# Optimization experiments

Hardware: AMD Instinct MI355X
Metric: run time of the kernel (lower is better)

## Reference

```python
import jax, jax.numpy as jnp
from jax import lax
import numpy as np

RPN_BBOX_STD_DEV = np.array([0.1, 0.1, 0.2, 0.2], dtype=np.float32)
PRE_NMS_LIMIT = 2048      # anchors kept before NMS (sorted by score)
NUM_PROPOSAL = 1000       # post-NMS proposal count (init kwarg num_proposal)
NMS_THRESHOLD = 0.7       # init kwarg nms_threshold


def setup_inputs() -> dict:
    key = jax.random.key(0)
    k1, k2, k3, k4, k5, k6 = jax.random.split(key, 6)
    B, N = 4, 1_000_000
    rpn_probs = jax.random.uniform(k1, (B, N, 2), dtype=jnp.float32)
    rpn_bbox = jax.random.normal(k2, (B, N, 4), dtype=jnp.float32)
    # well-formed normalized anchors (y1, x1, y2, x2)
    cy = jax.random.uniform(k3, (B, N), dtype=jnp.float32)
    cx = jax.random.uniform(k4, (B, N), dtype=jnp.float32)
    h = jax.random.uniform(k5, (B, N), dtype=jnp.float32) * 0.25 + 0.05
    w = jax.random.uniform(k6, (B, N), dtype=jnp.float32) * 0.25 + 0.05
    anchors = jnp.stack([cy - 0.5 * h, cx - 0.5 * w, cy + 0.5 * h, cx + 0.5 * w], axis=-1)
    return {"rpn_probs": rpn_probs, "rpn_bbox": rpn_bbox, "anchors": anchors}


def apply_box_deltas(boxes, deltas):
    # boxes: (..., 4) as (y1, x1, y2, x2); deltas: (dy, dx, log(dh), log(dw))
    h = boxes[..., 2] - boxes[..., 0]
    w = boxes[..., 3] - boxes[..., 1]
    cy = boxes[..., 0] + 0.5 * h + deltas[..., 0] * h
    cx = boxes[..., 1] + 0.5 * w + deltas[..., 1] * w
    h = h * jnp.exp(deltas[..., 2])
    w = w * jnp.exp(deltas[..., 3])
    return jnp.stack([cy - 0.5 * h, cx - 0.5 * w, cy + 0.5 * h, cx + 0.5 * w], axis=-1)


def pairwise_iou(boxes):
    # boxes: (P, 4) -> (P, P)
    y1, x1, y2, x2 = boxes[:, 0], boxes[:, 1], boxes[:, 2], boxes[:, 3]
    area = (y2 - y1) * (x2 - x1)
    ih = jnp.maximum(jnp.minimum(y2[:, None], y2[None, :]) - jnp.maximum(y1[:, None], y1[None, :]), 0.0)
    iw = jnp.maximum(jnp.minimum(x2[:, None], x2[None, :]) - jnp.maximum(x1[:, None], x1[None, :]), 0.0)
    inter = ih * iw
    union = area[:, None] + area[None, :] - inter
    return inter / (union + 1e-8)


def nms_single(boxes):
    # boxes (P, 4) sorted by score desc; greedy NMS then pad/clip to NUM_PROPOSAL
    P = boxes.shape[0]
    iou = pairwise_iou(boxes)
    idx = jnp.arange(P)

    def body(keep, i):
        suppress = keep[i] & (iou[i] > NMS_THRESHOLD) & (idx > i)
        return keep & ~suppress, None

    keep, _ = lax.scan(body, jnp.ones((P,), jnp.bool_), idx)
    rank = jnp.cumsum(keep) - 1                      # position among kept boxes
    valid = keep & (rank < NUM_PROPOSAL)
    pos = jnp.where(valid, rank, NUM_PROPOSAL)       # overflow row dropped below
    out = jnp.zeros((NUM_PROPOSAL + 1, 4), boxes.dtype).at[pos].set(
        jnp.where(valid[:, None], boxes, 0.0))
    return out[:NUM_PROPOSAL]


def reference(rpn_probs, rpn_bbox, anchors):
    scores = rpn_probs[:, :, 1]                                  # foreground prob (B, N)
    deltas = rpn_bbox * jnp.asarray(RPN_BBOX_STD_DEV)
    _, ix = lax.top_k(scores, PRE_NMS_LIMIT)                     # (B, P)
    deltas_top = jnp.take_along_axis(deltas, ix[..., None], axis=1)
    anchors_top = jnp.take_along_axis(anchors, ix[..., None], axis=1)
    boxes = apply_box_deltas(anchors_top, deltas_top)            # (B, P, 4)
    boxes = jnp.clip(boxes, 0.0, 1.0)                            # clip to [0,1] window
    proposals = jax.vmap(nms_single)(boxes)                      # (B, NUM_PROPOSAL, 4)
    return proposals
```

## Files before the change

### kernel.cpp

```cpp
#include <hip/hip_runtime.h>

#define B_ 4
#define N_ 1000000
#define K_ 2048
#define P_ 1000
#define CAP_ 8192
#define THR_ 0.7f
#define NF4_ 500000
#define META_STRIDE 32
#define TILE_ 512
#define NCH_ (CAP_ / TILE_)

#define OFF_HIST 0
#define OFF_META 1048576
#define OFF_COARSE (OFF_META + 1024)
#define OFF_CAND (OFF_COARSE + 4096)
#define OFF_TOPI (OFF_CAND + 262144)
#define OFF_BOX  (OFF_TOPI + 32768)
#define OFF_MASK (OFF_BOX + 131072)

__device__ __forceinline__ unsigned fkey(float f) {
  unsigned u = __float_as_uint(f);
  return (u & 0x80000000u) ? ~u : (u | 0x80000000u);
}

__device__ __forceinline__ unsigned long long readlane64(unsigned long long v, int l) {
  unsigned lo = (unsigned)__builtin_amdgcn_readlane((int)(unsigned)(v & 0xffffffffull), l);
  unsigned hi = (unsigned)__builtin_amdgcn_readlane((int)(unsigned)(v >> 32), l);
  return ((unsigned long long)hi << 32) | (unsigned long long)lo;
}

#define PIN16(k) asm volatile("" : "+v"(k[0]), "+v"(k[1]), "+v"(k[2]), "+v"(k[3]), \
                                   "+v"(k[4]), "+v"(k[5]), "+v"(k[6]), "+v"(k[7]), \
                                   "+v"(k[8]), "+v"(k[9]), "+v"(k[10]), "+v"(k[11]), \
                                   "+v"(k[12]), "+v"(k[13]), "+v"(k[14]), "+v"(k[15]))

__global__ void __launch_bounds__(1024) hist_kernel(const float4* __restrict__ probs4,
                                                    unsigned* __restrict__ hist) {
  int b = blockIdx.y;
  __shared__ unsigned h[32768];
  for (int i = threadIdx.x; i < 32768; i += 1024) h[i] = 0u;
  __syncthreads();
  const float4* p4 = probs4 + (size_t)b * NF4_;
  int base = blockIdx.x * 8192;
  float4 v[8];
#pragma unroll
  for (int c = 0; c < 8; ++c) {
    int i4 = base + c * 1024 + threadIdx.x;
    v[c] = (i4 < NF4_) ? p4[i4] : make_float4(0.f, 0.f, 0.f, 0.f);
  }
  unsigned k[16];
#pragma unroll
  for (int c = 0; c < 8; ++c) { k[2 * c] = fkey(v[c].y) >> 16; k[2 * c + 1] = fkey(v[c].w) >> 16; }
  PIN16(k);
#pragma unroll
  for (int c = 0; c < 8; ++c) {
    int i4 = base + c * 1024 + threadIdx.x;
    if (i4 < NF4_) {
      unsigned b0 = k[2 * c], b1 = k[2 * c + 1];
      atomicAdd(&h[b0 >> 1], 1u << ((b0 & 1u) << 4));
      atomicAdd(&h[b1 >> 1], 1u << ((b1 & 1u) << 4));
    }
  }
  __syncthreads();
  unsigned* g = hist + ((size_t)b << 16);
  for (int w = threadIdx.x; w < 32768; w += 1024) {
    unsigned x = h[w];
    if (x) {
      unsigned c0 = x & 0xFFFFu, c1 = x >> 16;
      if (c0) atomicAdd(&g[2 * w], c0);
      if (c1) atomicAdd(&g[2 * w + 1], c1);
    }
  }
}

__global__ void __launch_bounds__(64) coarse_kernel(const unsigned* __restrict__ hist,
                                                    unsigned* __restrict__ coarse) {
  int b = blockIdx.y, g = blockIdx.x, lane = threadIdx.x;
  const uint4* h4 = (const uint4*)(hist + (((size_t)b) << 16) + ((size_t)g << 8));
  uint4 v = h4[lane];
  unsigned s = v.x + v.y + v.z + v.w;
#pragma unroll
  for (int off = 32; off >= 1; off >>= 1) s += __shfl_xor(s, off, 64);
  if (lane == 0) coarse[b * 256 + g] = s;
}

__global__ void select_kernel(const unsigned* __restrict__ hist, const unsigned* __restrict__ coarse,
                              unsigned* __restrict__ meta) {
  int b = blockIdx.x, t = threadIdx.x;
  __shared__ unsigned suf[256];
  __shared__ int tc_s;
  __shared__ unsigned above_s;
  const unsigned* g = hist + ((size_t)b << 16);
  suf[t] = coarse[b * 256 + t];
  __syncthreads();
  for (int off = 1; off < 256; off <<= 1) {
    unsigned add = (t + off < 256) ? suf[t + off] : 0u;
    __syncthreads();
    suf[t] += add;
    __syncthreads();
  }
  unsigned nxt = (t < 255) ? suf[t + 1] : 0u;
  if (suf[t] >= K_ && (t == 255 || nxt < K_)) { tc_s = t; above_s = nxt; }
  __syncthreads();
  int tc = tc_s;
  unsigned above = above_s;
  unsigned bs = g[tc * 256 + t];
  __syncthreads();
  suf[t] = bs;
  __syncthreads();
  for (int off = 1; off < 256; off <<= 1) {
    unsigned add = (t + off < 256) ? suf[t + off] : 0u;
    __syncthreads();
    suf[t] += add;
    __syncthreads();
  }
  unsigned nxt2 = (t < 255) ? suf[t + 1] : 0u;
  if (above + suf[t] >= K_ && (t == 255 || above + nxt2 < K_))
    meta[b * META_STRIDE + 0] = (unsigned)(tc * 256 + t);
}

__global__ void __launch_bounds__(256) compact_kernel(const float4* __restrict__ probs4,
                                                      unsigned* __restrict__ meta,
                                                      uint2* __restrict__ cand) {
  int b = blockIdx.y;
  __shared__ unsigned lcnt, gbase_s;
  __shared__ uint2 buf[4096];
  if (threadIdx.x == 0) lcnt = 0u;
  __syncthreads();
  unsigned cb = meta[b * META_STRIDE + 0];
  const float4* p4 = probs4 + (size_t)b * NF4_;
  int base = blockIdx.x * 2048;
  int lane = threadIdx.x & 63;
  float4 v[8];
#pragma unroll
  for (int c = 0; c < 8; ++c) {
    int i4 = base + c * 256 + threadIdx.x;
    v[c] = (i4 < NF4_) ? p4[i4] : make_float4(0.f, 0.f, 0.f, 0.f);
  }
  unsigned k[16];
#pragma unroll
  for (int c = 0; c < 8; ++c) { k[2 * c] = fkey(v[c].y); k[2 * c + 1] = fkey(v[c].w); }
  PIN16(k);
#pragma unroll
  for (int c = 0; c < 8; ++c) {
#pragma unroll
    for (int s = 0; s < 2; ++s) {
      int i4 = base + c * 256 + threadIdx.x;
      unsigned key = k[2 * c + s];
      bool pass = (i4 < NF4_) && ((key >> 16) >= cb);
      unsigned long long m = __ballot(pass);
      if (m) {
        int leader = __ffsll(m) - 1;
        unsigned wbase = 0;
        if (lane == leader) wbase = atomicAdd(&lcnt, (unsigned)__popcll(m));
        wbase = __shfl(wbase, leader, 64);
        if (pass) {
          unsigned pos = wbase + (unsigned)__popcll(m & ((1ull << lane) - 1ull));
          buf[pos] = make_uint2(key, (unsigned)(2 * i4 + s));
        }
      }
    }
  }
  __syncthreads();
  unsigned cnt = lcnt;
  if (threadIdx.x == 0) gbase_s = atomicAdd(&meta[b * META_STRIDE + 1], cnt);
  __syncthreads();
  unsigned gbase = gbase_s;
  for (unsigned i = threadIdx.x; i < cnt; i += 256) {
    unsigned pos = gbase + i;
    if (pos < CAP_) cand[(size_t)b * CAP_ + pos] = buf[i];
  }
}

__global__ void __launch_bounds__(256) rank_kernel(const uint2* __restrict__ cand,
                                                   const unsigned* __restrict__ meta,
                                                   unsigned* __restrict__ partial) {
  int b = blockIdx.z;
  unsigned M = meta[b * META_STRIDE + 1];
  if (M > CAP_) M = CAP_;
  unsigned tb = blockIdx.y * TILE_;
  if (tb >= M) return;
  if ((unsigned)(blockIdx.x * 256) >= M) return;
  __shared__ __align__(16) uint2 tile[TILE_];
  unsigned n = M - tb;
  if (n > TILE_) n = TILE_;
  for (unsigned t = threadIdx.x; t < n; t += 256) tile[t] = cand[(size_t)b * CAP_ + tb + t];
  int ci = blockIdx.x * 256 + threadIdx.x;
  bool act = ci < (int)M;
  uint2 me = make_uint2(0u, 0u);
  if (act) me = cand[(size_t)b * CAP_ + ci];
  unsigned long long my = ((unsigned long long)me.x << 32) | (unsigned long long)(unsigned)(~me.y);
  __syncthreads();
  if (act) {
    unsigned rank = 0;
    unsigned n2 = n >> 1;
    const uint4* t4 = (const uint4*)tile;
    for (unsigned j = 0; j < n2; ++j) {
      uint4 v = t4[j];
      unsigned long long c0 = ((unsigned long long)v.x << 32) | (unsigned long long)(unsigned)(~v.y);
      unsigned long long c1 = ((unsigned long long)v.z << 32) | (unsigned long long)(unsigned)(~v.w);
      rank += (unsigned)(c0 > my) + (unsigned)(c1 > my);
    }
    if (n & 1) {
      uint2 v = tile[n - 1];
      unsigned long long c0 = ((unsigned long long)v.x << 32) | (unsigned long long)(unsigned)(~v.y);
      rank += (unsigned)(c0 > my);
    }
    partial[((size_t)b * NCH_ + blockIdx.y) * CAP_ + ci] = rank;
  }
}

__global__ void __launch_bounds__(256) scatter_kernel(const uint2* __restrict__ cand,
                                                      const unsigned* __restrict__ meta,
                                                      const unsigned* __restrict__ partial,
                                                      const float4* __restrict__ bbox,
                                                      const float4* __restrict__ anch,
                                                      float4* __restrict__ boxes) {
  int b = blockIdx.y;
  unsigned M = meta[b * META_STRIDE + 1];
  if (M > CAP_) M = CAP_;
  unsigned ci = blockIdx.x * 256 + threadIdx.x;
  if (ci >= M) return;
  unsigned nch = (M + TILE_ - 1) / TILE_;
  const unsigned* pp = partial + (size_t)b * NCH_ * CAP_ + ci;
  unsigned rank = 0;
  for (unsigned c = 0; c < nch; ++c) rank += pp[(size_t)c * CAP_];
  if (rank >= K_) return;
  unsigned idx = cand[(size_t)b * CAP_ + ci].y;
  size_t base = (size_t)b * N_ + idx;
  float4 a = anch[base];
  float4 d = bbox[base];
  float d0 = d.x * 0.1f, d1 = d.y * 0.1f, d2 = d.z * 0.2f, d3 = d.w * 0.2f;
  float h = a.z - a.x, w = a.w - a.y;
  float cy = (a.x + 0.5f * h) + d0 * h;
  float cx = (a.y + 0.5f * w) + d1 * w;
  float h2 = h * expf(d2);
  float w2 = w * expf(d3);
  float y1 = cy - 0.5f * h2, x1 = cx - 0.5f * w2;
  float y2 = cy + 0.5f * h2, x2 = cx + 0.5f * w2;
  y1 = fminf(fmaxf(y1, 0.f), 1.f);
  x1 = fminf(fmaxf(x1, 0.f), 1.f);
  y2 = fminf(fmaxf(y2, 0.f), 1.f);
  x2 = fminf(fmaxf(x2, 0.f), 1.f);
  boxes[(b << 11) + rank] = make_float4(y1, x1, y2, x2);
}

__global__ void mask_kernel(const float4* __restrict__ boxes, unsigned long long* __restrict__ mask) {
  int wid = blockIdx.x * 4 + (threadIdx.x >> 6);
  int lane = threadIdx.x & 63;
  int b = wid >> 12;
  int rb = (wid >> 5) & 127;
  int jb = wid & 31;
  if (jb < (rb >> 2)) return;
  int j = (jb << 6) + lane;
  float4 bj = boxes[(b << 11) + j];
  float areaJ = (bj.z - bj.x) * (bj.w - bj.y);
#pragma unroll
  for (int r = 0; r < 16; ++r) {
    int i = (rb << 4) + r;
    float4 bi = boxes[(b << 11) + i];
    float areaI = (bi.z - bi.x) * (bi.w - bi.y);
    float yA = fmaxf(bi.x, bj.x), xA = fmaxf(bi.y, bj.y);
    float yB = fminf(bi.z, bj.z), xB = fminf(bi.w, bj.w);
    float ih = fmaxf(yB - yA, 0.f), iw = fmaxf(xB - xA, 0.f);
    float inter = ih * iw;
    float uni = areaI + areaJ - inter;
    float iou = inter / (uni + 1e-8f);
    bool pred = (iou > THR_) && (j > i);
    unsigned long long bits = __ballot(pred);
    if (lane == 0) mask[((size_t)((b << 11) + i) << 5) + jb] = bits;
  }
}

__global__ void __launch_bounds__(64) nms_kernel(const unsigned long long* __restrict__ mask,
                                                 const float4* __restrict__ boxes,
                                                 float4* __restrict__ out) {
  int b = blockIdx.x;
  int lane = threadIdx.x;
  __shared__ unsigned long long rows[64][33];
  __shared__ unsigned long long keptm[32];
  __shared__ int pre[32];
  __shared__ short sel[P_];
  if (lane < 32) keptm[lane] = 0ull;
  for (int r = lane; r < P_; r += 64) sel[r] = -1;
  int w = lane & 31, half = lane >> 5;
  const unsigned long long* mbase = mask + (((size_t)(b << 11)) << 5);
  unsigned long long r0[32];
#pragma unroll
  for (int j = 0; j < 32; ++j) r0[j] = mbase[j * 64 + lane];
#pragma unroll
  for (int j = 0; j < 32; ++j) rows[2 * j + half][w] = r0[j];
  __syncthreads();
  unsigned long long rem = 0ull;
  int cnt = 0;
  for (int c = 0; c < 32; ++c) {
    bool pf = (c < 31) && (w > c);
    if (pf) {
      const unsigned long long* srcN = mbase + (((size_t)(c + 1)) << 11);
#pragma unroll
      for (int j = 0; j < 32; ++j) r0[j] = srcN[j * 64 + lane];
    }
    unsigned long long rin = rows[lane][c];
    unsigned long long cur = readlane64(rem, c);
    unsigned long long kept = 0ull;
#pragma unroll
    for (int k2 = 0; k2 < 64; ++k2) {
      unsigned long long rk = readlane64(rin, k2);
      unsigned long long alive = ((cur >> k2) & 1ull) ^ 1ull;
      cur |= rk & (0ull - alive);
      kept |= alive << k2;
    }
    if (lane == 0) keptm[c] = kept;
    cnt += (int)__popcll(kept);
    if (cnt >= P_) break;
    if (w > c) {
      unsigned long long acc = 0ull;
#pragma unroll
      for (int k2 = 0; k2 < 32; ++k2) {
        int row = half * 32 + k2;
        acc |= rows[row][w] & (0ull - ((kept >> row) & 1ull));
      }
      acc |= __shfl_xor(acc, 32, 64);
      rem |= acc;
    }
    if (pf) {
#pragma unroll
      for (int j = 0; j < 32; ++j) rows[2 * j + half][w] = r0[j];
    }
    __syncthreads();
  }
  __syncthreads();
  if (lane == 0) {
    int run = 0;
    for (int c = 0; c < 32; ++c) { pre[c] = run; run += (int)__popcll(keptm[c]); }
  }
  __syncthreads();
  for (int i = lane; i < K_; i += 64) {
    int c = i >> 6, k2 = i & 63;
    unsigned long long km = keptm[c];
    if ((km >> k2) & 1ull) {
      int rank = pre[c] + (int)__popcll(km & ((1ull << k2) - 1ull));
      if (rank < P_) sel[rank] = (short)i;
    }
  }
  __syncthreads();
  for (int r = lane; r < P_; r += 64) {
    int i = sel[r];
    float4 v = make_float4(0.f, 0.f, 0.f, 0.f);
    if (i >= 0) v = boxes[(b << 11) + i];
    out[b * P_ + r] = v;
  }
}

extern "C" void kernel_launch(void* const* d_in, const int* in_sizes, int n_in,
                              void* d_out, int out_size, void* d_ws, size_t ws_size,
                              hipStream_t stream) {
  const float4* probs4 = (const float4*)d_in[0];
  const float4* bbox   = (const float4*)d_in[1];
  const float4* anch   = (const float4*)d_in[2];
  char* ws = (char*)d_ws;
  unsigned* hist = (unsigned*)(ws + OFF_HIST);
  unsigned* meta = (unsigned*)(ws + OFF_META);
  unsigned* coarse = (unsigned*)(ws + OFF_COARSE);
  uint2* cand = (uint2*)(ws + OFF_CAND);
  float4* boxes = (float4*)(ws + OFF_BOX);
  unsigned long long* mask = (unsigned long long*)(ws + OFF_MASK);
  unsigned* partial = (unsigned*)(ws + OFF_MASK);
  float4* out = (float4*)d_out;

  hipMemsetAsync(ws, 0, OFF_COARSE, stream);

  hist_kernel<<<dim3(62, B_), 1024, 0, stream>>>(probs4, hist);
  coarse_kernel<<<dim3(256, B_), 64, 0, stream>>>(hist, coarse);
  select_kernel<<<B_, 256, 0, stream>>>(hist, coarse, meta);
  compact_kernel<<<dim3(245, B_), 256, 0, stream>>>(probs4, meta, cand);
  rank_kernel<<<dim3(CAP_ / 256, NCH_, B_), 256, 0, stream>>>(cand, meta, partial);
  scatter_kernel<<<dim3(CAP_ / 256, B_), 256, 0, stream>>>(cand, meta, partial, bbox, anch, boxes);
  mask_kernel<<<(B_ * 128 * 32) / 4, 256, 0, stream>>>(boxes, mask);
  nms_kernel<<<B_, 64, 0, stream>>>(mask, boxes, out);
}
```

Baseline: 255.1 us.

## Parallelize NMS sweep across four waves with double-buffered rows and sparse resolve

The NMS kernel grows from one wave to four. Each wave now prefetches 8 mask rows instead of 32, and the chunk rows are double-buffered in shared memory. Inside a chunk, the serial 64-step resolve is replaced by a ballot over nonzero rows that visits only rows with suppression bits. The running suppression state moves to shared memory and is updated with atomicOr from all waves. The cost is an extra block-wide barrier per chunk and some shared-memory atomics.

```diff
diff --git a/kernel.cpp b/kernel.cpp
--- a/kernel.cpp
+++ b/kernel.cpp
@@ -273,70 +273,87 @@
   }
 }
 
-__global__ void __launch_bounds__(64) nms_kernel(const unsigned long long* __restrict__ mask,
-                                                 const float4* __restrict__ boxes,
-                                                 float4* __restrict__ out) {
+__global__ void __launch_bounds__(256) nms_kernel(const unsigned long long* __restrict__ mask,
+                                                  const float4* __restrict__ boxes,
+                                                  float4* __restrict__ out) {
   int b = blockIdx.x;
-  int lane = threadIdx.x;
-  __shared__ unsigned long long rows[64][33];
+  int t = threadIdx.x;
+  int wid = t >> 6, lane = t & 63;
+  int w = lane & 31, half = lane >> 5;
+  __shared__ unsigned long long rows[2][64][33];
+  __shared__ unsigned long long remS[32];
   __shared__ unsigned long long keptm[32];
   __shared__ int pre[32];
   __shared__ short sel[P_];
-  if (lane < 32) keptm[lane] = 0ull;
-  for (int r = lane; r < P_; r += 64) sel[r] = -1;
-  int w = lane & 31, half = lane >> 5;
+  __shared__ int stopF;
+  if (t < 32) { remS[t] = 0ull; keptm[t] = 0ull; }
+  if (t == 0) stopF = 0;
+  for (int r = t; r < P_; r += 256) sel[r] = -1;
   const unsigned long long* mbase = mask + (((size_t)(b << 11)) << 5);
-  unsigned long long r0[32];
-#pragma unroll
-  for (int j = 0; j < 32; ++j) r0[j] = mbase[j * 64 + lane];
-#pragma unroll
-  for (int j = 0; j < 32; ++j) rows[2 * j + half][w] = r0[j];
-  __syncthreads();
-  unsigned long long rem = 0ull;
+  unsigned long long r0[8];
+  int rowb = 2 * wid + half;
+#pragma unroll
+  for (int j = 0; j < 8; ++j) r0[j] = mbase[j * 256 + t];
+#pragma unroll
+  for (int j = 0; j < 8; ++j) rows[0][8 * j + rowb][w] = r0[j];
+  __syncthreads();
+  int cb = 0;
   int cnt = 0;
   for (int c = 0; c < 32; ++c) {
     bool pf = (c < 31) && (w > c);
     if (pf) {
       const unsigned long long* srcN = mbase + (((size_t)(c + 1)) << 11);
 #pragma unroll
-      for (int j = 0; j < 32; ++j) r0[j] = srcN[j * 64 + lane];
-    }
-    unsigned long long rin = rows[lane][c];
-    unsigned long long cur = readlane64(rem, c);
-    unsigned long long kept = 0ull;
-#pragma unroll
-    for (int k2 = 0; k2 < 64; ++k2) {
-      unsigned long long rk = readlane64(rin, k2);
-      unsigned long long alive = ((cur >> k2) & 1ull) ^ 1ull;
-      cur |= rk & (0ull - alive);
-      kept |= alive << k2;
-    }
-    if (lane == 0) keptm[c] = kept;
-    cnt += (int)__popcll(kept);
-    if (cnt >= P_) break;
+      for (int j = 0; j < 8; ++j) r0[j] = srcN[j * 256 + t];
+    }
+    if (wid == 0) {
+      unsigned long long rin = rows[cb][lane][c];
+      unsigned long long cur = remS[c];
+      unsigned long long bm = __ballot(rin != 0ull);
+      while (bm) {
+        int k2 = __ffsll((long long)bm) - 1;
+        bm &= bm - 1;
+        if (!((cur >> k2) & 1ull)) cur |= readlane64(rin, k2);
+      }
+      unsigned long long kept = ~cur;
+      cnt += (int)__popcll(kept);
+      if (lane == 0) {
+        keptm[c] = kept;
+        if (cnt >= P_) stopF = 1;
+      }
+    }
+    __syncthreads();
+    if (stopF) break;
     if (w > c) {
+      unsigned long long kept = keptm[c];
       unsigned long long acc = 0ull;
 #pragma unroll
-      for (int k2 = 0; k2 < 32; ++k2) {
-        int row = half * 32 + k2;
-        acc |= rows[row][w] & (0ull - ((kept >> row) & 1ull));
+      for (int j = 0; j < 8; ++j) {
+        int row = 8 * j + rowb;
+        acc |= rows[cb][row][w] & (0ull - ((kept >> row) & 1ull));
       }
       acc |= __shfl_xor(acc, 32, 64);
-      rem |= acc;
+      if (half == 0) {
+        unsigned lo = (unsigned)acc, hi = (unsigned)(acc >> 32);
+        unsigned* rp = (unsigned*)&remS[w];
+        if (lo) atomicOr(rp, lo);
+        if (hi) atomicOr(rp + 1, hi);
+      }
     }
     if (pf) {
 #pragma unroll
-      for (int j = 0; j < 32; ++j) rows[2 * j + half][w] = r0[j];
-    }
-    __syncthreads();
-  }
-  __syncthreads();
-  if (lane == 0) {
+      for (int j = 0; j < 8; ++j) rows[cb ^ 1][8 * j + rowb][w] = r0[j];
+    }
+    __syncthreads();
+    cb ^= 1;
+  }
+  __syncthreads();
+  if (t == 0) {
     int run = 0;
     for (int c = 0; c < 32; ++c) { pre[c] = run; run += (int)__popcll(keptm[c]); }
   }
   __syncthreads();
-  for (int i = lane; i < K_; i += 64) {
+  for (int i = t; i < K_; i += 256) {
     int c = i >> 6, k2 = i & 63;
     unsigned long long km = keptm[c];
     if ((km >> k2) & 1ull) {
@@ -345,7 +362,7 @@
     }
   }
   __syncthreads();
-  for (int r = lane; r < P_; r += 64) {
+  for (int r = t; r < P_; r += 256) {
     int i = sel[r];
     float4 v = make_float4(0.f, 0.f, 0.f, 0.f);
     if (i >= 0) v = boxes[(b << 11) + i];
@@ -378,5 +395,5 @@
   rank_kernel<<<dim3(CAP_ / 256, NCH_, B_), 256, 0, stream>>>(cand, meta, partial);
   scatter_kernel<<<dim3(CAP_ / 256, B_), 256, 0, stream>>>(cand, meta, partial, bbox, anch, boxes);
   mask_kernel<<<(B_ * 128 * 32) / 4, 256, 0, stream>>>(boxes, mask);
-  nms_kernel<<<B_, 64, 0, stream>>>(mask, boxes, out);
-}
+  nms_kernel<<<B_, 256, 0, stream>>>(mask, boxes, out);
+}
```

Result: faster. 218.3 us (-14.4%).

## Shrink radix histogram, drop coarse pass, make NMS sparse over suppressing rows

Applied to the files above, without the earlier changes.

The histogram is cut to 16K clamped bins packed as 16-bit pairs, which removes the coarse kernel and shrinks the memset. The mask matrix is zeroed inside the hist kernel. The mask kernel now writes only nonzero words and records per-row 'any suppression' bits. NMS walks only rows that can suppress something, instead of scanning all 2048 rows bit by bit. This trades fewer launches and less serial work for some atomics, and bins are coarse near the clamp boundaries. Clamping keys below 0x8000 is fine because all probabilities are non-negative.

```diff
diff --git a/kernel.cpp b/kernel.cpp
--- a/kernel.cpp
+++ b/kernel.cpp
@@ -12,16 +12,22 @@
 #define NCH_ (CAP_ / TILE_)
 
 #define OFF_HIST 0
-#define OFF_META 1048576
-#define OFF_COARSE (OFF_META + 1024)
-#define OFF_CAND (OFF_COARSE + 4096)
-#define OFF_TOPI (OFF_CAND + 262144)
-#define OFF_BOX  (OFF_TOPI + 32768)
-#define OFF_MASK (OFF_BOX + 131072)
+#define OFF_META 131072
+#define OFF_ROWANY 132096
+#define OFF_CAND 133120
+#define OFF_BOX  395264
+#define OFF_MASK 526336
+#define OFF_PART 2623488
 
 __device__ __forceinline__ unsigned fkey(float f) {
   unsigned u = __float_as_uint(f);
   return (u & 0x80000000u) ? ~u : (u | 0x80000000u);
+}
+
+__device__ __forceinline__ int b16of(unsigned key) {
+  int x = (int)(key >> 16) - 0x8000;
+  x = x < 0 ? 0 : x;
+  return x > 0x3FFF ? 0x3FFF : x;
 }
 
 __device__ __forceinline__ unsigned long long readlane64(unsigned long long v, int l) {
@@ -35,27 +41,38 @@
                                    "+v"(k[8]), "+v"(k[9]), "+v"(k[10]), "+v"(k[11]), \
                                    "+v"(k[12]), "+v"(k[13]), "+v"(k[14]), "+v"(k[15]))
 
-__global__ void __launch_bounds__(1024) hist_kernel(const float4* __restrict__ probs4,
-                                                    unsigned* __restrict__ hist) {
+__global__ void __launch_bounds__(512) hist_kernel(const float4* __restrict__ probs4,
+                                                   unsigned* __restrict__ hist,
+                                                   uint4* __restrict__ maskz) {
   int b = blockIdx.y;
-  __shared__ unsigned h[32768];
-  for (int i = threadIdx.x; i < 32768; i += 1024) h[i] = 0u;
+  __shared__ unsigned h[8192];
+  for (int i = threadIdx.x; i < 8192; i += 512) h[i] = 0u;
+  {
+    unsigned gid = (unsigned)(b * 124 + blockIdx.x);
+    if (threadIdx.x < 320u) {
+      unsigned zi = gid * 320u + threadIdx.x;
+      if (zi < 131072u) maskz[zi] = make_uint4(0u, 0u, 0u, 0u);
+    }
+  }
   __syncthreads();
   const float4* p4 = probs4 + (size_t)b * NF4_;
-  int base = blockIdx.x * 8192;
+  int base = blockIdx.x * 4096;
   float4 v[8];
 #pragma unroll
   for (int c = 0; c < 8; ++c) {
-    int i4 = base + c * 1024 + threadIdx.x;
+    int i4 = base + c * 512 + threadIdx.x;
     v[c] = (i4 < NF4_) ? p4[i4] : make_float4(0.f, 0.f, 0.f, 0.f);
   }
   unsigned k[16];
 #pragma unroll
-  for (int c = 0; c < 8; ++c) { k[2 * c] = fkey(v[c].y) >> 16; k[2 * c + 1] = fkey(v[c].w) >> 16; }
+  for (int c = 0; c < 8; ++c) {
+    k[2 * c] = (unsigned)b16of(fkey(v[c].y));
+    k[2 * c + 1] = (unsigned)b16of(fkey(v[c].w));
+  }
   PIN16(k);
 #pragma unroll
   for (int c = 0; c < 8; ++c) {
-    int i4 = base + c * 1024 + threadIdx.x;
+    int i4 = base + c * 512 + threadIdx.x;
     if (i4 < NF4_) {
       unsigned b0 = k[2 * c], b1 = k[2 * c + 1];
       atomicAdd(&h[b0 >> 1], 1u << ((b0 & 1u) << 4));
@@ -63,49 +80,49 @@
     }
   }
   __syncthreads();
-  unsigned* g = hist + ((size_t)b << 16);
-  for (int w = threadIdx.x; w < 32768; w += 1024) {
+  unsigned* g = hist + b * 8192;
+  for (int w = threadIdx.x; w < 8192; w += 512) {
     unsigned x = h[w];
-    if (x) {
-      unsigned c0 = x & 0xFFFFu, c1 = x >> 16;
-      if (c0) atomicAdd(&g[2 * w], c0);
-      if (c1) atomicAdd(&g[2 * w + 1], c1);
-    }
-  }
-}
-
-__global__ void __launch_bounds__(64) coarse_kernel(const unsigned* __restrict__ hist,
-                                                    unsigned* __restrict__ coarse) {
-  int b = blockIdx.y, g = blockIdx.x, lane = threadIdx.x;
-  const uint4* h4 = (const uint4*)(hist + (((size_t)b) << 16) + ((size_t)g << 8));
-  uint4 v = h4[lane];
-  unsigned s = v.x + v.y + v.z + v.w;
-#pragma unroll
-  for (int off = 32; off >= 1; off >>= 1) s += __shfl_xor(s, off, 64);
-  if (lane == 0) coarse[b * 256 + g] = s;
-}
-
-__global__ void select_kernel(const unsigned* __restrict__ hist, const unsigned* __restrict__ coarse,
-                              unsigned* __restrict__ meta) {
+    if (x) atomicAdd(&g[w], x);
+  }
+}
+
+__global__ void select_kernel(const unsigned* __restrict__ hist, unsigned* __restrict__ meta) {
   int b = blockIdx.x, t = threadIdx.x;
+  const unsigned* g = hist + b * 8192;
+  __shared__ unsigned part[256];
+  __shared__ unsigned gsum[64];
   __shared__ unsigned suf[256];
   __shared__ int tc_s;
   __shared__ unsigned above_s;
-  const unsigned* g = hist + ((size_t)b << 16);
-  suf[t] = coarse[b * 256 + t];
-  __syncthreads();
-  for (int off = 1; off < 256; off <<= 1) {
-    unsigned add = (t + off < 256) ? suf[t + off] : 0u;
-    __syncthreads();
-    suf[t] += add;
-    __syncthreads();
-  }
-  unsigned nxt = (t < 255) ? suf[t + 1] : 0u;
-  if (suf[t] >= K_ && (t == 255 || nxt < K_)) { tc_s = t; above_s = nxt; }
+  {
+    int grp = t >> 2, q = t & 3;
+    const unsigned* p = g + grp * 128 + q * 32;
+    unsigned s = 0;
+#pragma unroll 8
+    for (int i = 0; i < 32; ++i) { unsigned x = p[i]; s += (x & 0xFFFFu) + (x >> 16); }
+    part[t] = s;
+  }
+  __syncthreads();
+  if (t < 64) gsum[t] = part[4 * t] + part[4 * t + 1] + part[4 * t + 2] + part[4 * t + 3];
+  __syncthreads();
+  if (t < 64) suf[t] = gsum[t];
+  __syncthreads();
+  for (int off = 1; off < 64; off <<= 1) {
+    unsigned add = (t < 64 && t + off < 64) ? suf[t + off] : 0u;
+    __syncthreads();
+    if (t < 64) suf[t] += add;
+    __syncthreads();
+  }
+  if (t < 64) {
+    unsigned nxt = (t < 63) ? suf[t + 1] : 0u;
+    if (suf[t] >= K_ && (t == 63 || nxt < K_)) { tc_s = t; above_s = nxt; }
+  }
   __syncthreads();
   int tc = tc_s;
   unsigned above = above_s;
-  unsigned bs = g[tc * 256 + t];
+  unsigned wv = g[tc * 128 + (t >> 1)];
+  unsigned bs = (t & 1) ? (wv >> 16) : (wv & 0xFFFFu);
   __syncthreads();
   suf[t] = bs;
   __syncthreads();
@@ -128,7 +145,7 @@
   __shared__ uint2 buf[4096];
   if (threadIdx.x == 0) lcnt = 0u;
   __syncthreads();
-  unsigned cb = meta[b * META_STRIDE + 0];
+  int cb = (int)meta[b * META_STRIDE + 0];
   const float4* p4 = probs4 + (size_t)b * NF4_;
   int base = blockIdx.x * 2048;
   int lane = threadIdx.x & 63;
@@ -148,7 +165,7 @@
     for (int s = 0; s < 2; ++s) {
       int i4 = base + c * 256 + threadIdx.x;
       unsigned key = k[2 * c + s];
-      bool pass = (i4 < NF4_) && ((key >> 16) >= cb);
+      bool pass = (i4 < NF4_) && (b16of(key) >= cb);
       unsigned long long m = __ballot(pass);
       if (m) {
         int leader = __ffsll(m) - 1;
@@ -246,7 +263,8 @@
   boxes[(b << 11) + rank] = make_float4(y1, x1, y2, x2);
 }
 
-__global__ void mask_kernel(const float4* __restrict__ boxes, unsigned long long* __restrict__ mask) {
+__global__ void mask_kernel(const float4* __restrict__ boxes, unsigned long long* __restrict__ mask,
+                            unsigned long long* __restrict__ rowAny) {
   int wid = blockIdx.x * 4 + (threadIdx.x >> 6);
   int lane = threadIdx.x & 63;
   int b = wid >> 12;
@@ -269,76 +287,81 @@
     float iou = inter / (uni + 1e-8f);
     bool pred = (iou > THR_) && (j > i);
     unsigned long long bits = __ballot(pred);
-    if (lane == 0) mask[((size_t)((b << 11) + i) << 5) + jb] = bits;
+    if (bits && lane == 0) {
+      mask[((size_t)((b << 11) + i) << 5) + jb] = bits;
+      atomicOr(&rowAny[b * 32 + (i >> 6)], 1ull << (i & 63));
+    }
   }
 }
 
 __global__ void __launch_bounds__(64) nms_kernel(const unsigned long long* __restrict__ mask,
+                                                 const unsigned long long* __restrict__ rowAny,
                                                  const float4* __restrict__ boxes,
                                                  float4* __restrict__ out) {
   int b = blockIdx.x;
   int lane = threadIdx.x;
-  __shared__ unsigned long long rows[64][33];
-  __shared__ unsigned long long keptm[32];
+  int w = lane & 31;
+  __shared__ unsigned long long rowsBuf[256][32];
+  __shared__ unsigned short evRow[2048];
+  __shared__ unsigned long long keptw[32];
   __shared__ int pre[32];
   __shared__ short sel[P_];
-  if (lane < 32) keptm[lane] = 0ull;
   for (int r = lane; r < P_; r += 64) sel[r] = -1;
-  int w = lane & 31, half = lane >> 5;
-  const unsigned long long* mbase = mask + (((size_t)(b << 11)) << 5);
-  unsigned long long r0[32];
-#pragma unroll
-  for (int j = 0; j < 32; ++j) r0[j] = mbase[j * 64 + lane];
-#pragma unroll
-  for (int j = 0; j < 32; ++j) rows[2 * j + half][w] = r0[j];
-  __syncthreads();
-  unsigned long long rem = 0ull;
-  int cnt = 0;
-  for (int c = 0; c < 32; ++c) {
-    bool pf = (c < 31) && (w > c);
-    if (pf) {
-      const unsigned long long* srcN = mbase + (((size_t)(c + 1)) << 11);
-#pragma unroll
-      for (int j = 0; j < 32; ++j) r0[j] = srcN[j * 64 + lane];
-    }
-    unsigned long long rin = rows[lane][c];
-    unsigned long long cur = readlane64(rem, c);
-    unsigned long long kept = 0ull;
-#pragma unroll
-    for (int k2 = 0; k2 < 64; ++k2) {
-      unsigned long long rk = readlane64(rin, k2);
-      unsigned long long alive = ((cur >> k2) & 1ull) ^ 1ull;
-      cur |= rk & (0ull - alive);
-      kept |= alive << k2;
-    }
-    if (lane == 0) keptm[c] = kept;
-    cnt += (int)__popcll(kept);
-    if (cnt >= P_) break;
-    if (w > c) {
-      unsigned long long acc = 0ull;
-#pragma unroll
-      for (int k2 = 0; k2 < 32; ++k2) {
-        int row = half * 32 + k2;
-        acc |= rows[row][w] & (0ull - ((kept >> row) & 1ull));
-      }
-      acc |= __shfl_xor(acc, 32, 64);
-      rem |= acc;
-    }
-    if (pf) {
-#pragma unroll
-      for (int j = 0; j < 32; ++j) rows[2 * j + half][w] = r0[j];
-    }
-    __syncthreads();
-  }
+  unsigned long long anyv = (lane < 32) ? rowAny[b * 32 + lane] : 0ull;
+  unsigned pc = (unsigned)__popcll(anyv);
+  unsigned pref = pc;
+#pragma unroll
+  for (int off = 1; off < 32; off <<= 1) {
+    unsigned tv = __shfl_up(pref, off, 64);
+    if ((lane & 31) >= off) pref += tv;
+  }
+  int E = __shfl((int)pref, 31, 64);
+  if (lane < 32) {
+    unsigned o = pref - pc;
+    unsigned long long bm = anyv;
+    while (bm) {
+      int i = __ffsll((long long)bm) - 1;
+      bm &= bm - 1;
+      evRow[o++] = (unsigned short)((lane << 6) + i);
+    }
+  }
+  __syncthreads();
+  unsigned long long sup = 0ull;
+  const unsigned long long* mb = mask + (((size_t)(b << 11)) << 5);
+  for (int eb = 0; eb < E; eb += 256) {
+    int ne = E - eb;
+    if (ne > 256) ne = 256;
+    for (int k = (lane >> 5); k < ne; k += 2) {
+      int r = evRow[eb + k];
+      rowsBuf[k][w] = mb[((size_t)r << 5) + w];
+    }
+    __syncthreads();
+    int i0 = evRow[eb];
+    unsigned long long v0 = rowsBuf[0][w];
+    int i1 = 0;
+    unsigned long long v1 = 0ull;
+    if (ne > 1) { i1 = evRow[eb + 1]; v1 = rowsBuf[1][w]; }
+    for (int e = 0; e < ne; ++e) {
+      int i2 = 0;
+      unsigned long long v2 = 0ull;
+      if (e + 2 < ne) { i2 = evRow[eb + e + 2]; v2 = rowsBuf[e + 2][w]; }
+      int wi = i0 >> 6;
+      unsigned long long sw = readlane64(sup, wi);
+      if (!((sw >> (i0 & 63)) & 1ull)) sup |= v0;
+      i0 = i1; v0 = v1; i1 = i2; v1 = v2;
+    }
+    __syncthreads();
+  }
+  if (lane < 32) keptw[lane] = ~sup;
   __syncthreads();
   if (lane == 0) {
     int run = 0;
-    for (int c = 0; c < 32; ++c) { pre[c] = run; run += (int)__popcll(keptm[c]); }
+    for (int c = 0; c < 32; ++c) { pre[c] = run; run += (int)__popcll(keptw[c]); }
   }
   __syncthreads();
   for (int i = lane; i < K_; i += 64) {
     int c = i >> 6, k2 = i & 63;
-    unsigned long long km = keptm[c];
+    unsigned long long km = keptw[c];
     if ((km >> k2) & 1ull) {
       int rank = pre[c] + (int)__popcll(km & ((1ull << k2) - 1ull));
       if (rank < P_) sel[rank] = (short)i;
@@ -362,21 +385,20 @@
   char* ws = (char*)d_ws;
   unsigned* hist = (unsigned*)(ws + OFF_HIST);
   unsigned* meta = (unsigned*)(ws + OFF_META);
-  unsigned* coarse = (unsigned*)(ws + OFF_COARSE);
+  unsigned long long* rowAny = (unsigned long long*)(ws + OFF_ROWANY);
   uint2* cand = (uint2*)(ws + OFF_CAND);
   float4* boxes = (float4*)(ws + OFF_BOX);
   unsigned long long* mask = (unsigned long long*)(ws + OFF_MASK);
-  unsigned* partial = (unsigned*)(ws + OFF_MASK);
+  unsigned* partial = (unsigned*)(ws + OFF_PART);
   float4* out = (float4*)d_out;
 
-  hipMemsetAsync(ws, 0, OFF_COARSE, stream);
-
-  hist_kernel<<<dim3(62, B_), 1024, 0, stream>>>(probs4, hist);
-  coarse_kernel<<<dim3(256, B_), 64, 0, stream>>>(hist, coarse);
-  select_kernel<<<B_, 256, 0, stream>>>(hist, coarse, meta);
+  hipMemsetAsync(ws, 0, OFF_CAND, stream);
+
+  hist_kernel<<<dim3(124, B_), 512, 0, stream>>>(probs4, hist, (uint4*)mask);
+  select_kernel<<<B_, 256, 0, stream>>>(hist, meta);
   compact_kernel<<<dim3(245, B_), 256, 0, stream>>>(probs4, meta, cand);
   rank_kernel<<<dim3(CAP_ / 256, NCH_, B_), 256, 0, stream>>>(cand, meta, partial);
   scatter_kernel<<<dim3(CAP_ / 256, B_), 256, 0, stream>>>(cand, meta, partial, bbox, anch, boxes);
-  mask_kernel<<<(B_ * 128 * 32) / 4, 256, 0, stream>>>(boxes, mask);
-  nms_kernel<<<B_, 64, 0, stream>>>(mask, boxes, out);
-}
+  mask_kernel<<<(B_ * 128 * 32) / 4, 256, 0, stream>>>(boxes, mask, rowAny);
+  nms_kernel<<<B_, 64, 0, stream>>>(mask, rowAny, boxes, out);
+}
```

After: 306.5 us. +20.2%, slower.

## Fuse coarse/select and rank/scatter kernels, sparse-scan NMS serial step

Applied to the files above, without the earlier changes.

Merges the coarse histogram reduction into a single 1024-thread select kernel that sums 64-bin groups directly. Fuses rank and scatter by accumulating ranks atomically into a zeroed buffer and letting the last finishing block per batch (via a completion counter) perform the box decode and scatter. Replaces the fixed 64-step serial NMS scan with a loop over only the rows that have nonzero overlap bits and are not already suppressed. This removes two kernel launches and the partial-rank buffer, but adds a larger memset, global atomics, and a single-block tail that serializes the scatter per batch.

```diff
diff --git a/kernel.cpp b/kernel.cpp
--- a/kernel.cpp
+++ b/kernel.cpp
@@ -9,15 +9,16 @@
 #define NF4_ 500000
 #define META_STRIDE 32
 #define TILE_ 512
-#define NCH_ (CAP_ / TILE_)
+#define RNB 32
+#define RNT 16
 
 #define OFF_HIST 0
 #define OFF_META 1048576
-#define OFF_COARSE (OFF_META + 1024)
-#define OFF_CAND (OFF_COARSE + 4096)
-#define OFF_TOPI (OFF_CAND + 262144)
-#define OFF_BOX  (OFF_TOPI + 32768)
-#define OFF_MASK (OFF_BOX + 131072)
+#define OFF_RANKTOT 1049600
+#define OFF_CAND 1180672
+#define OFF_BOX  1442816
+#define OFF_MASK 1573888
+#define MEMSET_BYTES OFF_CAND
 
 __device__ __forceinline__ unsigned fkey(float f) {
   unsigned u = __float_as_uint(f);
@@ -74,50 +75,43 @@
   }
 }
 
-__global__ void __launch_bounds__(64) coarse_kernel(const unsigned* __restrict__ hist,
-                                                    unsigned* __restrict__ coarse) {
-  int b = blockIdx.y, g = blockIdx.x, lane = threadIdx.x;
-  const uint4* h4 = (const uint4*)(hist + (((size_t)b) << 16) + ((size_t)g << 8));
-  uint4 v = h4[lane];
-  unsigned s = v.x + v.y + v.z + v.w;
-#pragma unroll
-  for (int off = 32; off >= 1; off >>= 1) s += __shfl_xor(s, off, 64);
-  if (lane == 0) coarse[b * 256 + g] = s;
-}
-
-__global__ void select_kernel(const unsigned* __restrict__ hist, const unsigned* __restrict__ coarse,
-                              unsigned* __restrict__ meta) {
+__global__ void __launch_bounds__(1024) select_kernel(const unsigned* __restrict__ hist,
+                                                      unsigned* __restrict__ meta) {
   int b = blockIdx.x, t = threadIdx.x;
-  __shared__ unsigned suf[256];
-  __shared__ int tc_s;
+  const unsigned* g = hist + ((size_t)b << 16);
+  __shared__ unsigned suf[1024];
+  __shared__ int tg_s;
   __shared__ unsigned above_s;
-  const unsigned* g = hist + ((size_t)b << 16);
-  suf[t] = coarse[b * 256 + t];
-  __syncthreads();
-  for (int off = 1; off < 256; off <<= 1) {
-    unsigned add = (t + off < 256) ? suf[t + off] : 0u;
+  {
+    const uint4* p = (const uint4*)g + t * 16;
+    unsigned s = 0;
+#pragma unroll
+    for (int i = 0; i < 16; ++i) { uint4 v = p[i]; s += v.x + v.y + v.z + v.w; }
+    suf[t] = s;
+  }
+  __syncthreads();
+  for (int off = 1; off < 1024; off <<= 1) {
+    unsigned add = (t + off < 1024) ? suf[t + off] : 0u;
     __syncthreads();
     suf[t] += add;
     __syncthreads();
   }
-  unsigned nxt = (t < 255) ? suf[t + 1] : 0u;
-  if (suf[t] >= K_ && (t == 255 || nxt < K_)) { tc_s = t; above_s = nxt; }
-  __syncthreads();
-  int tc = tc_s;
+  unsigned nxt = (t < 1023) ? suf[t + 1] : 0u;
+  if (suf[t] >= K_ && (t == 1023 || nxt < K_)) { tg_s = t; above_s = nxt; }
+  __syncthreads();
+  int tg = tg_s;
   unsigned above = above_s;
-  unsigned bs = g[tc * 256 + t];
-  __syncthreads();
-  suf[t] = bs;
-  __syncthreads();
-  for (int off = 1; off < 256; off <<= 1) {
-    unsigned add = (t + off < 256) ? suf[t + off] : 0u;
-    __syncthreads();
-    suf[t] += add;
-    __syncthreads();
-  }
-  unsigned nxt2 = (t < 255) ? suf[t + 1] : 0u;
-  if (above + suf[t] >= K_ && (t == 255 || above + nxt2 < K_))
-    meta[b * META_STRIDE + 0] = (unsigned)(tc * 256 + t);
+  if (t < 64) {
+    unsigned cb = g[tg * 64 + t];
+    unsigned s2 = cb;
+#pragma unroll
+    for (int off = 1; off < 64; off <<= 1) {
+      unsigned v = __shfl_down(s2, off, 64);
+      if (t + off < 64) s2 += v;
+    }
+    if (above + s2 >= K_ && (t == 63 || above + (s2 - cb) < K_))
+      meta[b * META_STRIDE + 0] = (unsigned)(tg * 64 + t);
+  }
 }
 
 __global__ void __launch_bounds__(256) compact_kernel(const float4* __restrict__ probs4,
@@ -174,76 +168,76 @@
 }
 
 __global__ void __launch_bounds__(256) rank_kernel(const uint2* __restrict__ cand,
-                                                   const unsigned* __restrict__ meta,
-                                                   unsigned* __restrict__ partial) {
+                                                   unsigned* __restrict__ meta,
+                                                   unsigned* __restrict__ rankTot,
+                                                   const float4* __restrict__ bbox,
+                                                   const float4* __restrict__ anch,
+                                                   float4* __restrict__ boxes) {
   int b = blockIdx.z;
   unsigned M = meta[b * META_STRIDE + 1];
   if (M > CAP_) M = CAP_;
   unsigned tb = blockIdx.y * TILE_;
-  if (tb >= M) return;
-  if ((unsigned)(blockIdx.x * 256) >= M) return;
   __shared__ __align__(16) uint2 tile[TILE_];
-  unsigned n = M - tb;
-  if (n > TILE_) n = TILE_;
-  for (unsigned t = threadIdx.x; t < n; t += 256) tile[t] = cand[(size_t)b * CAP_ + tb + t];
-  int ci = blockIdx.x * 256 + threadIdx.x;
-  bool act = ci < (int)M;
-  uint2 me = make_uint2(0u, 0u);
-  if (act) me = cand[(size_t)b * CAP_ + ci];
-  unsigned long long my = ((unsigned long long)me.x << 32) | (unsigned long long)(unsigned)(~me.y);
-  __syncthreads();
-  if (act) {
-    unsigned rank = 0;
-    unsigned n2 = n >> 1;
-    const uint4* t4 = (const uint4*)tile;
-    for (unsigned j = 0; j < n2; ++j) {
-      uint4 v = t4[j];
-      unsigned long long c0 = ((unsigned long long)v.x << 32) | (unsigned long long)(unsigned)(~v.y);
-      unsigned long long c1 = ((unsigned long long)v.z << 32) | (unsigned long long)(unsigned)(~v.w);
-      rank += (unsigned)(c0 > my) + (unsigned)(c1 > my);
-    }
-    if (n & 1) {
-      uint2 v = tile[n - 1];
-      unsigned long long c0 = ((unsigned long long)v.x << 32) | (unsigned long long)(unsigned)(~v.y);
-      rank += (unsigned)(c0 > my);
-    }
-    partial[((size_t)b * NCH_ + blockIdx.y) * CAP_ + ci] = rank;
-  }
-}
-
-__global__ void __launch_bounds__(256) scatter_kernel(const uint2* __restrict__ cand,
-                                                      const unsigned* __restrict__ meta,
-                                                      const unsigned* __restrict__ partial,
-                                                      const float4* __restrict__ bbox,
-                                                      const float4* __restrict__ anch,
-                                                      float4* __restrict__ boxes) {
-  int b = blockIdx.y;
-  unsigned M = meta[b * META_STRIDE + 1];
-  if (M > CAP_) M = CAP_;
-  unsigned ci = blockIdx.x * 256 + threadIdx.x;
-  if (ci >= M) return;
-  unsigned nch = (M + TILE_ - 1) / TILE_;
-  const unsigned* pp = partial + (size_t)b * NCH_ * CAP_ + ci;
-  unsigned rank = 0;
-  for (unsigned c = 0; c < nch; ++c) rank += pp[(size_t)c * CAP_];
-  if (rank >= K_) return;
-  unsigned idx = cand[(size_t)b * CAP_ + ci].y;
-  size_t base = (size_t)b * N_ + idx;
-  float4 a = anch[base];
-  float4 d = bbox[base];
-  float d0 = d.x * 0.1f, d1 = d.y * 0.1f, d2 = d.z * 0.2f, d3 = d.w * 0.2f;
-  float h = a.z - a.x, w = a.w - a.y;
-  float cy = (a.x + 0.5f * h) + d0 * h;
-  float cx = (a.y + 0.5f * w) + d1 * w;
-  float h2 = h * expf(d2);
-  float w2 = w * expf(d3);
-  float y1 = cy - 0.5f * h2, x1 = cx - 0.5f * w2;
-  float y2 = cy + 0.5f * h2, x2 = cx + 0.5f * w2;
-  y1 = fminf(fmaxf(y1, 0.f), 1.f);
-  x1 = fminf(fmaxf(x1, 0.f), 1.f);
-  y2 = fminf(fmaxf(y2, 0.f), 1.f);
-  x2 = fminf(fmaxf(x2, 0.f), 1.f);
-  boxes[(b << 11) + rank] = make_float4(y1, x1, y2, x2);
+  __shared__ int last_s;
+  bool blkActive = (tb < M) && ((unsigned)(blockIdx.x * 256) < M);
+  if (blkActive) {
+    unsigned n = M - tb;
+    if (n > TILE_) n = TILE_;
+    for (unsigned t = threadIdx.x; t < n; t += 256) tile[t] = cand[(size_t)b * CAP_ + tb + t];
+    int ci = blockIdx.x * 256 + threadIdx.x;
+    bool act = ci < (int)M;
+    uint2 me = make_uint2(0u, 0u);
+    if (act) me = cand[(size_t)b * CAP_ + ci];
+    unsigned long long my = ((unsigned long long)me.x << 32) | (unsigned long long)(unsigned)(~me.y);
+    __syncthreads();
+    if (act) {
+      unsigned rank = 0;
+      unsigned n2 = n >> 1;
+      const uint4* t4 = (const uint4*)tile;
+      for (unsigned j = 0; j < n2; ++j) {
+        uint4 v = t4[j];
+        unsigned long long c0 = ((unsigned long long)v.x << 32) | (unsigned long long)(unsigned)(~v.y);
+        unsigned long long c1 = ((unsigned long long)v.z << 32) | (unsigned long long)(unsigned)(~v.w);
+        rank += (unsigned)(c0 > my) + (unsigned)(c1 > my);
+      }
+      if (n & 1) {
+        uint2 v = tile[n - 1];
+        unsigned long long c0 = ((unsigned long long)v.x << 32) | (unsigned long long)(unsigned)(~v.y);
+        rank += (unsigned)(c0 > my);
+      }
+      if (rank) atomicAdd(&rankTot[(size_t)b * CAP_ + ci], rank);
+    }
+  }
+  __syncthreads();
+  if (threadIdx.x == 0) {
+    __threadfence();
+    last_s = (atomicAdd(&meta[b * META_STRIDE + 2], 1u) == (unsigned)(RNB * RNT - 1));
+  }
+  __syncthreads();
+  if (!last_s) return;
+  __threadfence();
+  for (unsigned ci = threadIdx.x; ci < M; ci += 256) {
+    unsigned rank = __hip_atomic_load(&rankTot[(size_t)b * CAP_ + ci],
+                                      __ATOMIC_RELAXED, __HIP_MEMORY_SCOPE_AGENT);
+    if (rank >= K_) continue;
+    unsigned idx = cand[(size_t)b * CAP_ + ci].y;
+    size_t base = (size_t)b * N_ + idx;
+    float4 a = anch[base];
+    float4 d = bbox[base];
+    float d0 = d.x * 0.1f, d1 = d.y * 0.1f, d2 = d.z * 0.2f, d3 = d.w * 0.2f;
+    float h = a.z - a.x, w = a.w - a.y;
+    float cy = (a.x + 0.5f * h) + d0 * h;
+    float cx = (a.y + 0.5f * w) + d1 * w;
+    float h2 = h * expf(d2);
+    float w2 = w * expf(d3);
+    float y1 = cy - 0.5f * h2, x1 = cx - 0.5f * w2;
+    float y2 = cy + 0.5f * h2, x2 = cx + 0.5f * w2;
+    y1 = fminf(fmaxf(y1, 0.f), 1.f);
+    x1 = fminf(fmaxf(x1, 0.f), 1.f);
+    y2 = fminf(fmaxf(y2, 0.f), 1.f);
+    x2 = fminf(fmaxf(x2, 0.f), 1.f);
+    boxes[(b << 11) + rank] = make_float4(y1, x1, y2, x2);
+  }
 }
 
 __global__ void mask_kernel(const float4* __restrict__ boxes, unsigned long long* __restrict__ mask) {
@@ -278,13 +272,13 @@
                                                  float4* __restrict__ out) {
   int b = blockIdx.x;
   int lane = threadIdx.x;
+  int w = lane & 31, half = lane >> 5;
   __shared__ unsigned long long rows[64][33];
   __shared__ unsigned long long keptm[32];
   __shared__ int pre[32];
   __shared__ short sel[P_];
   if (lane < 32) keptm[lane] = 0ull;
   for (int r = lane; r < P_; r += 64) sel[r] = -1;
-  int w = lane & 31, half = lane >> 5;
   const unsigned long long* mbase = mask + (((size_t)(b << 11)) << 5);
   unsigned long long r0[32];
 #pragma unroll
@@ -303,14 +297,16 @@
     }
     unsigned long long rin = rows[lane][c];
     unsigned long long cur = readlane64(rem, c);
-    unsigned long long kept = 0ull;
-#pragma unroll
-    for (int k2 = 0; k2 < 64; ++k2) {
-      unsigned long long rk = readlane64(rin, k2);
-      unsigned long long alive = ((cur >> k2) & 1ull) ^ 1ull;
-      cur |= rk & (0ull - alive);
-      kept |= alive << k2;
-    }
+    unsigned long long bm = __ballot(rin != 0ull) & ~cur;
+    while (bm) {
+      int k2 = __ffsll((long long)bm) - 1;
+      bm &= bm - 1;
+      if (!((cur >> k2) & 1ull)) {
+        cur |= readlane64(rin, k2);
+        bm &= ~cur;
+      }
+    }
+    unsigned long long kept = ~cur;
     if (lane == 0) keptm[c] = kept;
     cnt += (int)__popcll(kept);
     if (cnt >= P_) break;
@@ -362,21 +358,18 @@
   char* ws = (char*)d_ws;
   unsigned* hist = (unsigned*)(ws + OFF_HIST);
   unsigned* meta = (unsigned*)(ws + OFF_META);
-  unsigned* coarse = (unsigned*)(ws + OFF_COARSE);
+  unsigned* rankTot = (unsigned*)(ws + OFF_RANKTOT);
   uint2* cand = (uint2*)(ws + OFF_CAND);
   float4* boxes = (float4*)(ws + OFF_BOX);
   unsigned long long* mask = (unsigned long long*)(ws + OFF_MASK);
-  unsigned* partial = (unsigned*)(ws + OFF_MASK);
   float4* out = (float4*)d_out;
 
-  hipMemsetAsync(ws, 0, OFF_COARSE, stream);
+  hipMemsetAsync(ws, 0, MEMSET_BYTES, stream);
 
   hist_kernel<<<dim3(62, B_), 1024, 0, stream>>>(probs4, hist);
-  coarse_kernel<<<dim3(256, B_), 64, 0, stream>>>(hist, coarse);
-  select_kernel<<<B_, 256, 0, stream>>>(hist, coarse, meta);
+  select_kernel<<<B_, 1024, 0, stream>>>(hist, meta);
   compact_kernel<<<dim3(245, B_), 256, 0, stream>>>(probs4, meta, cand);
-  rank_kernel<<<dim3(CAP_ / 256, NCH_, B_), 256, 0, stream>>>(cand, meta, partial);
-  scatter_kernel<<<dim3(CAP_ / 256, B_), 256, 0, stream>>>(cand, meta, partial, bbox, anch, boxes);
+  rank_kernel<<<dim3(RNB, RNT, B_), 256, 0, stream>>>(cand, meta, rankTot, bbox, anch, boxes);
   mask_kernel<<<(B_ * 128 * 32) / 4, 256, 0, stream>>>(boxes, mask);
   nms_kernel<<<B_, 64, 0, stream>>>(mask, boxes, out);
 }
```

Result: slower. 304.7 us (+19.4%).
